# Optimization experiments

Hardware: AMD Instinct MI355X
Metric: run time of the kernel (lower is better)

## Reference

```python
import jax, jax.numpy as jnp
import numpy as np


def setup_inputs() -> dict:
    key = jax.random.key(0)
    kq, kk, kv, km = jax.random.split(key, 4)
    B, H, S, D = 2, 16, 2048, 64
    Q = jax.random.normal(kq, (B, H, S, D), dtype=jnp.float32)
    K = jax.random.normal(kk, (B, H, S, D), dtype=jnp.float32)
    V = jax.random.normal(kv, (B, H, S, D), dtype=jnp.float32)
    attn_mask = jax.random.randint(km, (B, 1, S, S), 0, 2, dtype=jnp.int32)
    return {"Q": Q, "K": K, "V": V, "attn_mask": attn_mask}


def reference(Q, K, V, attn_mask):
    d_k = jnp.asarray(K.shape[-1], dtype=Q.dtype)
    # scores: [B,H,S,S]
    scores = jnp.einsum("bhqd,bhkd->bhqk", Q, K) / jnp.sqrt(d_k)
    scores = jnp.where(attn_mask == 0, jnp.asarray(-1e9, scores.dtype), scores)
    attn_weights = jax.nn.softmax(scores, axis=-1)
    context = jnp.einsum("bhqk,bhkd->bhqd", attn_weights, V)
    return context, attn_weights
```

## Files before the change

kernel.cpp:

```cpp
#include <hip/hip_runtime.h>
#include <hip/hip_bf16.h>

typedef __attribute__((ext_vector_type(8))) short      short8;
typedef __attribute__((ext_vector_type(4))) float      floatx4;
typedef unsigned long long u64;
typedef unsigned short     u16;

#define DI __device__ __forceinline__

constexpr int BB = 2, HH = 16, SS = 2048, DD = 64;
constexpr int TK  = 64;
constexpr int NKT = SS / TK;
constexpr int PW  = 68;

constexpr size_t NELEM  = (size_t)BB * HH * SS * DD;
constexpr size_t OFF_VT = NELEM * 2;
constexpr size_t OFF_MB = OFF_VT + NELEM * 2;
constexpr size_t NWORDS = (size_t)BB * SS * (SS / 64);

DI u16 f2bfu(float f) {
    __hip_bfloat16 h = __float2bfloat16(f);
    return __builtin_bit_cast(u16, h);
}

DI short8 pack8(floatx4 a, floatx4 b) {
    short8 r;
    r[0] = (short)f2bfu(a[0]); r[1] = (short)f2bfu(a[1]);
    r[2] = (short)f2bfu(a[2]); r[3] = (short)f2bfu(a[3]);
    r[4] = (short)f2bfu(b[0]); r[5] = (short)f2bfu(b[1]);
    r[6] = (short)f2bfu(b[2]); r[7] = (short)f2bfu(b[3]);
    return r;
}

DI short8 cvt8s(const float* __restrict__ p, float s) {
    floatx4 a = *(const floatx4*)p;
    floatx4 b = *(const floatx4*)(p + 4);
    a *= s; b *= s;
    return pack8(a, b);
}

constexpr int KBLK = 2048;
constexpr int VBLK = 1024;
constexpr int MBLK = 4096;

__global__ __launch_bounds__(256)
void prep_kernel(const float* __restrict__ K, const float* __restrict__ V,
                 const int* __restrict__ mask,
                 u16* __restrict__ Kb, u16* __restrict__ Vt, u64* __restrict__ Mb)
{
    const int bx = (int)blockIdx.x, tid = (int)threadIdx.x;
    if (bx < KBLK) {
        size_t i = ((size_t)bx * 256 + tid) * 8;
        floatx4 a = *(const floatx4*)(K + i);
        floatx4 b = *(const floatx4*)(K + i + 4);
        *(short8*)(Kb + i) = pack8(a, b);
    } else if (bx < KBLK + VBLK) {
        __shared__ __align__(16) u16 T[DD * 72];
        const int idx = bx - KBLK;
        const int bh = idx >> 5, kt = idx & 31;
        const int kvr = tid >> 2, d0 = (tid & 3) * 16;
        const float* vp = V + ((size_t)bh * SS + kt * 64 + kvr) * DD + d0;
        floatx4 v0 = *(const floatx4*)vp;
        floatx4 v1 = *(const floatx4*)(vp + 4);
        floatx4 v2 = *(const floatx4*)(vp + 8);
        floatx4 v3 = *(const floatx4*)(vp + 12);
#pragma unroll
        for (int i = 0; i < 4; ++i) T[(d0 + i)      * 72 + kvr] = f2bfu(v0[i]);
#pragma unroll
        for (int i = 0; i < 4; ++i) T[(d0 + 4 + i)  * 72 + kvr] = f2bfu(v1[i]);
#pragma unroll
        for (int i = 0; i < 4; ++i) T[(d0 + 8 + i)  * 72 + kvr] = f2bfu(v2[i]);
#pragma unroll
        for (int i = 0; i < 4; ++i) T[(d0 + 12 + i) * 72 + kvr] = f2bfu(v3[i]);
        __syncthreads();
        const int d = tid >> 2, seg = (tid & 3) * 16;
        short8 s0 = *(const short8*)&T[d * 72 + seg];
        short8 s1 = *(const short8*)&T[d * 72 + seg + 8];
        u16* op = Vt + ((size_t)bh * DD + d) * SS + kt * 64 + seg;
        *(short8*)op       = s0;
        *(short8*)(op + 8) = s1;
    } else {
        const int mc = bx - (KBLK + VBLK);
        const int wv = tid >> 6, lane = tid & 63;
        const size_t gw = (size_t)mc * 4 + wv;
#pragma unroll
        for (int it = 0; it < 8; ++it) {
            size_t word = gw * 8 + it;
            int b   = (int)(word >> 16);
            int rem = (int)(word & 65535);
            int q = rem >> 5, wj = rem & 31;
            int v = mask[((size_t)b * SS + q) * SS + wj * 64 + lane];
            u64 bal = __ballot(v != 0);
            if (lane == 0) Mb[word] = bal;
        }
    }
}

__global__ __launch_bounds__(64, 4)
void sdpa_main(const float* __restrict__ Q,
               const u16*   __restrict__ Kb,
               const u16*   __restrict__ Vt,
               const u64*   __restrict__ Mb,
               float*       __restrict__ out_ctx,
               float*       __restrict__ out_w)
{
    __shared__ __align__(16) float Pw[16 * PW];

    const int lane = (int)threadIdx.x;
    const int quad = lane >> 4;
    const int col  = lane & 15;

    const int bh = (int)blockIdx.y;
    const int b  = bh >> 4;
    const int q0 = (int)blockIdx.x * 16;

    const size_t head = (size_t)bh * SS * DD;
    const u16* Kh = Kb + head;
    const u16* Vh = Vt + head;
    const u64* Mh = Mb + ((size_t)b * SS + q0) * (SS / 64);
    float*     Wh = out_w + (size_t)bh * SS * SS;

    short8 aQ0, aQ1;
    {
        const float* qp = Q + head + (size_t)(q0 + col) * DD + quad * 8;
        aQ0 = cvt8s(qp, 0.125f);
        aQ1 = cvt8s(qp + 32, 0.125f);
    }

    float mrow[4], lrow[4];
#pragma unroll
    for (int r = 0; r < 4; ++r) { mrow[r] = -__builtin_inff(); lrow[r] = 0.f; }

    for (int kt = 0; kt < NKT; ++kt) {
        const int kv0 = kt * TK;
        floatx4 acc[4];
#pragma unroll
        for (int nt = 0; nt < 4; ++nt) {
            const u16* kp = Kh + (size_t)(kv0 + nt * 16 + col) * DD + quad * 8;
            short8 b0 = *(const short8*)kp;
            short8 b1 = *(const short8*)(kp + 32);
            floatx4 a = {0.f, 0.f, 0.f, 0.f};
            a = __builtin_amdgcn_mfma_f32_16x16x32_bf16(aQ0, b0, a, 0, 0, 0);
            a = __builtin_amdgcn_mfma_f32_16x16x32_bf16(aQ1, b1, a, 0, 0, 0);
            acc[nt] = a;
        }
#pragma unroll
        for (int r = 0; r < 4; ++r) {
            const int rloc = quad * 4 + r;
            const u64 mw = Mh[(size_t)rloc * (SS / 64) + kt];
            float s[4];
#pragma unroll
            for (int nt = 0; nt < 4; ++nt) {
                unsigned mnt = (unsigned)(mw >> (nt * 16));
                s[nt] = ((mnt >> col) & 1u) ? acc[nt][r] : -1e9f;
            }
            float lm = fmaxf(fmaxf(s[0], s[1]), fmaxf(s[2], s[3]));
            float mn = fmaxf(mrow[r], lm);
            float p  = __expf(s[0] - mn) + __expf(s[1] - mn) + __expf(s[2] - mn) + __expf(s[3] - mn);
            lrow[r]  = lrow[r] * __expf(mrow[r] - mn) + p;
            mrow[r]  = mn;
        }
    }
#pragma unroll
    for (int r = 0; r < 4; ++r) {
#pragma unroll
        for (int off = 1; off < 16; off <<= 1) {
            float mo = __shfl_xor(mrow[r], off);
            float lo = __shfl_xor(lrow[r], off);
            float mn = fmaxf(mrow[r], mo);
            lrow[r] = lrow[r] * __expf(mrow[r] - mn) + lo * __expf(mo - mn);
            mrow[r] = mn;
        }
    }
    float rl[4];
#pragma unroll
    for (int r = 0; r < 4; ++r) rl[r] = 1.0f / lrow[r];

    floatx4 ctx[4];
#pragma unroll
    for (int nt = 0; nt < 4; ++nt) ctx[nt] = floatx4{0.f, 0.f, 0.f, 0.f};

    for (int kt = 0; kt < NKT; ++kt) {
        const int kv0 = kt * TK;

        floatx4 acc[4];
#pragma unroll
        for (int nt = 0; nt < 4; ++nt) {
            const u16* kp = Kh + (size_t)(kv0 + nt * 16 + col) * DD + quad * 8;
            short8 b0 = *(const short8*)kp;
            short8 b1 = *(const short8*)(kp + 32);
            floatx4 a = {0.f, 0.f, 0.f, 0.f};
            a = __builtin_amdgcn_mfma_f32_16x16x32_bf16(aQ0, b0, a, 0, 0, 0);
            a = __builtin_amdgcn_mfma_f32_16x16x32_bf16(aQ1, b1, a, 0, 0, 0);
            acc[nt] = a;
        }

#pragma unroll
        for (int r = 0; r < 4; ++r) {
            const int rloc = quad * 4 + r;
            const u64 mw = Mh[(size_t)rloc * (SS / 64) + kt];
#pragma unroll
            for (int nt = 0; nt < 4; ++nt) {
                unsigned mnt = (unsigned)(mw >> (nt * 16));
                float sv = ((mnt >> col) & 1u) ? acc[nt][r] : -1e9f;
                Pw[rloc * PW + nt * 16 + col] = __expf(sv - mrow[r]) * rl[r];
            }
        }
        __syncthreads();

        floatx4 pf0 = *(const floatx4*)&Pw[col * PW + quad * 8];
        floatx4 pf1 = *(const floatx4*)&Pw[col * PW + quad * 8 + 4];
        floatx4 pf2 = *(const floatx4*)&Pw[col * PW + 32 + quad * 8];
        floatx4 pf3 = *(const floatx4*)&Pw[col * PW + 32 + quad * 8 + 4];
        short8 pA0 = pack8(pf0, pf1);
        short8 pA1 = pack8(pf2, pf3);

#pragma unroll
        for (int i = 0; i < 4; ++i) {
            const int wr = (lane >> 4) + i * 4;
            const int c4 = (lane & 15) * 4;
            floatx4 wv = *(const floatx4*)&Pw[wr * PW + c4];
            __builtin_nontemporal_store(wv, (floatx4*)(Wh + (size_t)(q0 + wr) * SS + kv0 + c4));
        }

#pragma unroll
        for (int nt = 0; nt < 4; ++nt) {
            const u16* vp = Vh + (size_t)(nt * 16 + col) * SS + kv0 + quad * 8;
            short8 vB0 = *(const short8*)vp;
            short8 vB1 = *(const short8*)(vp + 32);
            ctx[nt] = __builtin_amdgcn_mfma_f32_16x16x32_bf16(pA0, vB0, ctx[nt], 0, 0, 0);
            ctx[nt] = __builtin_amdgcn_mfma_f32_16x16x32_bf16(pA1, vB1, ctx[nt], 0, 0, 0);
        }
        __syncthreads();
    }

#pragma unroll
    for (int nt = 0; nt < 4; ++nt) {
#pragma unroll
        for (int r = 0; r < 4; ++r) {
            const int q = q0 + quad * 4 + r;
            __builtin_nontemporal_store(ctx[nt][r],
                out_ctx + head + (size_t)q * DD + nt * 16 + col);
        }
    }
}

extern "C" void kernel_launch(void* const* d_in, const int* in_sizes, int n_in,
                              void* d_out, int out_size, void* d_ws, size_t ws_size,
                              hipStream_t stream) {
    const float* Q = (const float*)d_in[0];
    const float* K = (const float*)d_in[1];
    const float* V = (const float*)d_in[2];
    const int* mask = (const int*)d_in[3];

    float* out     = (float*)d_out;
    float* out_ctx = out;
    float* out_w   = out + (size_t)BB * HH * SS * DD;

    u16* Kb = (u16*)d_ws;
    u16* Vt = (u16*)((char*)d_ws + OFF_VT);
    u64* Mb = (u64*)((char*)d_ws + OFF_MB);
    (void)ws_size;

    hipLaunchKernelGGL(prep_kernel, dim3(KBLK + VBLK + MBLK), dim3(256), 0, stream,
                       K, V, mask, Kb, Vt, Mb);
    hipLaunchKernelGGL(sdpa_main, dim3(SS / 16, BB * HH), dim3(64), 0, stream,
                       Q, Kb, Vt, Mb, out_ctx, out_w);
}
```

Baseline: 889.2 us.

## Prefetch K/V tiles, store bf16 P in double-buffered LDS, remap blocks for XCD locality

Software-pipelines the K loads one tile ahead in both passes, hoists mask loads, and interleaves V loads with score computation. P is written directly as bf16 into a double-buffered LDS tile, which removes the two __syncthreads per iteration (one wave per block) and the fp32 LDS round trip. Attention weights are now stored straight from registers with per-element nontemporal stores instead of vectorised float4 stores. The grid is flattened and remapped so consecutive blocks on the same XCD share heads, and s_setprio wraps the MFMAs. The risks are narrower weight stores and higher register pressure.

```diff
diff --git a/kernel.cpp b/kernel.cpp
--- a/kernel.cpp
+++ b/kernel.cpp
@@ -11,12 +11,11 @@
 constexpr int BB = 2, HH = 16, SS = 2048, DD = 64;
 constexpr int TK  = 64;
 constexpr int NKT = SS / TK;
-constexpr int PW  = 68;
+constexpr int PB  = 72;
 
 constexpr size_t NELEM  = (size_t)BB * HH * SS * DD;
 constexpr size_t OFF_VT = NELEM * 2;
 constexpr size_t OFF_MB = OFF_VT + NELEM * 2;
-constexpr size_t NWORDS = (size_t)BB * SS * (SS / 64);
 
 DI u16 f2bfu(float f) {
     __hip_bfloat16 h = __float2bfloat16(f);
@@ -104,15 +103,17 @@
                float*       __restrict__ out_ctx,
                float*       __restrict__ out_w)
 {
-    __shared__ __align__(16) float Pw[16 * PW];
+    __shared__ __align__(16) u16 Pb[2 * 16 * PB];
 
     const int lane = (int)threadIdx.x;
     const int quad = lane >> 4;
     const int col  = lane & 15;
 
-    const int bh = (int)blockIdx.y;
-    const int b  = bh >> 4;
-    const int q0 = (int)blockIdx.x * 16;
+    const int id  = (int)blockIdx.x;
+    const int nid = (id & 7) * 512 + (id >> 3);
+    const int bh  = nid >> 7;
+    const int q0  = (nid & 127) * 16;
+    const int b   = bh >> 4;
 
     const size_t head = (size_t)bh * SS * DD;
     const u16* Kh = Kb + head;
@@ -127,31 +128,48 @@
         aQ1 = cvt8s(qp + 32, 0.125f);
     }
 
+    short8 kA[4], kB[4];
+#pragma unroll
+    for (int nt = 0; nt < 4; ++nt) {
+        const u16* kp = Kh + (size_t)(nt * 16 + col) * DD + quad * 8;
+        kA[nt] = *(const short8*)kp;
+        kB[nt] = *(const short8*)(kp + 32);
+    }
+
     float mrow[4], lrow[4];
 #pragma unroll
     for (int r = 0; r < 4; ++r) { mrow[r] = -__builtin_inff(); lrow[r] = 0.f; }
 
     for (int kt = 0; kt < NKT; ++kt) {
-        const int kv0 = kt * TK;
+        u64 mw[4];
+#pragma unroll
+        for (int r = 0; r < 4; ++r) mw[r] = Mh[(size_t)(quad * 4 + r) * (SS / 64) + kt];
+
         floatx4 acc[4];
-#pragma unroll
-        for (int nt = 0; nt < 4; ++nt) {
-            const u16* kp = Kh + (size_t)(kv0 + nt * 16 + col) * DD + quad * 8;
-            short8 b0 = *(const short8*)kp;
-            short8 b1 = *(const short8*)(kp + 32);
+        __builtin_amdgcn_s_setprio(1);
+#pragma unroll
+        for (int nt = 0; nt < 4; ++nt) {
             floatx4 a = {0.f, 0.f, 0.f, 0.f};
-            a = __builtin_amdgcn_mfma_f32_16x16x32_bf16(aQ0, b0, a, 0, 0, 0);
-            a = __builtin_amdgcn_mfma_f32_16x16x32_bf16(aQ1, b1, a, 0, 0, 0);
+            a = __builtin_amdgcn_mfma_f32_16x16x32_bf16(aQ0, kA[nt], a, 0, 0, 0);
+            a = __builtin_amdgcn_mfma_f32_16x16x32_bf16(aQ1, kB[nt], a, 0, 0, 0);
             acc[nt] = a;
         }
+        __builtin_amdgcn_s_setprio(0);
+
+        const int ktn = (kt + 1) & (NKT - 1);
+#pragma unroll
+        for (int nt = 0; nt < 4; ++nt) {
+            const u16* kp = Kh + (size_t)(ktn * TK + nt * 16 + col) * DD + quad * 8;
+            kA[nt] = *(const short8*)kp;
+            kB[nt] = *(const short8*)(kp + 32);
+        }
+
 #pragma unroll
         for (int r = 0; r < 4; ++r) {
-            const int rloc = quad * 4 + r;
-            const u64 mw = Mh[(size_t)rloc * (SS / 64) + kt];
             float s[4];
 #pragma unroll
             for (int nt = 0; nt < 4; ++nt) {
-                unsigned mnt = (unsigned)(mw >> (nt * 16));
+                unsigned mnt = (unsigned)(mw[r] >> (nt * 16));
                 s[nt] = ((mnt >> col) & 1u) ? acc[nt][r] : -1e9f;
             }
             float lm = fmaxf(fmaxf(s[0], s[1]), fmaxf(s[2], s[3]));
@@ -182,56 +200,59 @@
 
     for (int kt = 0; kt < NKT; ++kt) {
         const int kv0 = kt * TK;
-
-        floatx4 acc[4];
-#pragma unroll
-        for (int nt = 0; nt < 4; ++nt) {
-            const u16* kp = Kh + (size_t)(kv0 + nt * 16 + col) * DD + quad * 8;
-            short8 b0 = *(const short8*)kp;
-            short8 b1 = *(const short8*)(kp + 32);
+        u16* Pl = &Pb[(kt & 1) * (16 * PB)];
+
+        u64 mw[4];
+#pragma unroll
+        for (int r = 0; r < 4; ++r) mw[r] = Mh[(size_t)(quad * 4 + r) * (SS / 64) + kt];
+
+        const int ktn = (kt + 1) & (NKT - 1);
+        short8 vA[4], vB[4];
+
+#pragma unroll
+        for (int nt = 0; nt < 4; ++nt) {
             floatx4 a = {0.f, 0.f, 0.f, 0.f};
-            a = __builtin_amdgcn_mfma_f32_16x16x32_bf16(aQ0, b0, a, 0, 0, 0);
-            a = __builtin_amdgcn_mfma_f32_16x16x32_bf16(aQ1, b1, a, 0, 0, 0);
-            acc[nt] = a;
-        }
-
-#pragma unroll
-        for (int r = 0; r < 4; ++r) {
-            const int rloc = quad * 4 + r;
-            const u64 mw = Mh[(size_t)rloc * (SS / 64) + kt];
-#pragma unroll
-            for (int nt = 0; nt < 4; ++nt) {
-                unsigned mnt = (unsigned)(mw >> (nt * 16));
-                float sv = ((mnt >> col) & 1u) ? acc[nt][r] : -1e9f;
-                Pw[rloc * PW + nt * 16 + col] = __expf(sv - mrow[r]) * rl[r];
-            }
-        }
-        __syncthreads();
-
-        floatx4 pf0 = *(const floatx4*)&Pw[col * PW + quad * 8];
-        floatx4 pf1 = *(const floatx4*)&Pw[col * PW + quad * 8 + 4];
-        floatx4 pf2 = *(const floatx4*)&Pw[col * PW + 32 + quad * 8];
-        floatx4 pf3 = *(const floatx4*)&Pw[col * PW + 32 + quad * 8 + 4];
-        short8 pA0 = pack8(pf0, pf1);
-        short8 pA1 = pack8(pf2, pf3);
-
-#pragma unroll
-        for (int i = 0; i < 4; ++i) {
-            const int wr = (lane >> 4) + i * 4;
-            const int c4 = (lane & 15) * 4;
-            floatx4 wv = *(const floatx4*)&Pw[wr * PW + c4];
-            __builtin_nontemporal_store(wv, (floatx4*)(Wh + (size_t)(q0 + wr) * SS + kv0 + c4));
-        }
-
-#pragma unroll
-        for (int nt = 0; nt < 4; ++nt) {
-            const u16* vp = Vh + (size_t)(nt * 16 + col) * SS + kv0 + quad * 8;
-            short8 vB0 = *(const short8*)vp;
-            short8 vB1 = *(const short8*)(vp + 32);
-            ctx[nt] = __builtin_amdgcn_mfma_f32_16x16x32_bf16(pA0, vB0, ctx[nt], 0, 0, 0);
-            ctx[nt] = __builtin_amdgcn_mfma_f32_16x16x32_bf16(pA1, vB1, ctx[nt], 0, 0, 0);
-        }
-        __syncthreads();
+            __builtin_amdgcn_s_setprio(1);
+            a = __builtin_amdgcn_mfma_f32_16x16x32_bf16(aQ0, kA[nt], a, 0, 0, 0);
+            a = __builtin_amdgcn_mfma_f32_16x16x32_bf16(aQ1, kB[nt], a, 0, 0, 0);
+            __builtin_amdgcn_s_setprio(0);
+
+            {
+                const u16* kp = Kh + (size_t)(ktn * TK + nt * 16 + col) * DD + quad * 8;
+                kA[nt] = *(const short8*)kp;
+                kB[nt] = *(const short8*)(kp + 32);
+            }
+            {
+                const u16* vp = Vh + (size_t)(nt * 16 + col) * SS + kv0 + quad * 8;
+                vA[nt] = *(const short8*)vp;
+                vB[nt] = *(const short8*)(vp + 32);
+            }
+
+#pragma unroll
+            for (int r = 0; r < 4; ++r) {
+                const int rloc = quad * 4 + r;
+                unsigned mnt = (unsigned)(mw[r] >> (nt * 16));
+                float sv = ((mnt >> col) & 1u) ? a[r] : -1e9f;
+                float w  = __expf(sv - mrow[r]) * rl[r];
+                __builtin_nontemporal_store(w,
+                    Wh + (size_t)(q0 + rloc) * SS + kv0 + nt * 16 + col);
+                Pl[rloc * PB + nt * 16 + col] = f2bfu(w);
+            }
+        }
+
+        asm volatile("s_waitcnt lgkmcnt(0)" ::: "memory");
+        __builtin_amdgcn_sched_barrier(0);
+
+        short8 pA0 = *(const short8*)&Pl[col * PB + quad * 8];
+        short8 pA1 = *(const short8*)&Pl[col * PB + 32 + quad * 8];
+
+        __builtin_amdgcn_s_setprio(1);
+#pragma unroll
+        for (int nt = 0; nt < 4; ++nt) {
+            ctx[nt] = __builtin_amdgcn_mfma_f32_16x16x32_bf16(pA0, vA[nt], ctx[nt], 0, 0, 0);
+            ctx[nt] = __builtin_amdgcn_mfma_f32_16x16x32_bf16(pA1, vB[nt], ctx[nt], 0, 0, 0);
+        }
+        __builtin_amdgcn_s_setprio(0);
     }
 
 #pragma unroll
@@ -264,6 +285,6 @@
 
     hipLaunchKernelGGL(prep_kernel, dim3(KBLK + VBLK + MBLK), dim3(256), 0, stream,
                        K, V, mask, Kb, Vt, Mb);
-    hipLaunchKernelGGL(sdpa_main, dim3(SS / 16, BB * HH), dim3(64), 0, stream,
+    hipLaunchKernelGGL(sdpa_main, dim3(SS / 16 * BB * HH), dim3(64), 0, stream,
                        Q, Kb, Vt, Mb, out_ctx, out_w);
 }
```

Result: slower. 964.8 us (+8.5%).
